# Kernel tuning notes

Hardware: AMD Instinct MI355X
Metric: run time of the kernel (lower is better)

Reference implementation:

```python
import jax, jax.numpy as jnp
import numpy as np

WIDE = 15
PAD = (WIDE - 1) // 2
FREQS = np.array([1., 2., 3., 4., 5., 6.], dtype=np.float32)  # wave_base_ml frequencies


def _lstm_dir(x, wih, whh, b):
    # x: [B,T,F]; wih: [4H,F]; whh: [4H,H]; b: [4H] (b_ih+b_hh fused)
    H = whh.shape[1]
    xg = jnp.einsum('btf,gf->btg', x, wih) + b  # precompute input projections
    def step(carry, xt):
        h, c = carry
        g = xt + h @ whh.T
        i, f, gg, o = jnp.split(g, 4, axis=-1)  # torch gate order i,f,g,o
        c = jax.nn.sigmoid(f) * c + jax.nn.sigmoid(i) * jnp.tanh(gg)
        h = jax.nn.sigmoid(o) * jnp.tanh(c)
        return (h, c), h
    h0 = jnp.zeros((x.shape[0], H), x.dtype)
    _, hs = jax.lax.scan(step, (h0, h0), jnp.swapaxes(xg, 0, 1))
    return jnp.swapaxes(hs, 0, 1)


def _bn(x, g, b, eps=1e-5):
    # training-mode BatchNorm1d over (N, L) per channel; x: [B,C,L]
    m = jnp.mean(x, axis=(0, 2), keepdims=True)
    v = jnp.var(x, axis=(0, 2), keepdims=True)
    return (x - m) * jax.lax.rsqrt(v + eps) * g[None, :, None] + b[None, :, None]


def _conv1d(x, w, b):
    y = jax.lax.conv_general_dilated(x, w, (1,), 'VALID', dimension_numbers=('NCH', 'OIH', 'NCH'))
    return y + b[None, :, None]


def _haar(x):
    s = 0.7071067811865476
    return (x[..., ::2] + x[..., 1::2]) * s, (x[..., ::2] - x[..., 1::2]) * s


def _forward(x, lstm_wif, lstm_whf, lstm_bf, lstm_wir, lstm_whr, lstm_br, base_w, base_b,
             g1, be1, g2, be2, g3, be3, g4, be4, g5, be5,
             w2, b2, w3, b3, w4, b4, w5, b5, fcw, fcb):
    xt = jnp.swapaxes(x, 1, 2)  # [B,T,F]
    fwd = _lstm_dir(xt, lstm_wif, lstm_whf, lstm_bf)
    bwd = _lstm_dir(xt[:, ::-1], lstm_wir, lstm_whr, lstm_br)[:, ::-1]
    X = jnp.swapaxes(jnp.concatenate([fwd, bwd], axis=-1), 1, 2)  # [B,C,T], C=2*dim
    B, C, T = X.shape
    Xp = jnp.pad(X, ((0, 0), (0, 0), (PAD, PAD)))
    # shared sliding windows [B,C,T,WIDE] used both for scale conv and Furi_conv
    Xwin = jnp.stack([Xp[..., k:k + T] for k in range(WIDE)], axis=-1)
    offs = (jnp.arange(WIDE, dtype=X.dtype) - PAD) / WIDE
    outs = []
    for ii in range(len(FREQS)):
        scales = jax.nn.relu(jnp.einsum('bctk,k->bct', Xwin, base_w[ii]) + base_b[ii])
        # per-position cosine Fourier basis generated from the learned scales
        bases = jnp.cos((2.0 * np.pi * FREQS[ii]) * scales[..., None] * offs)  # [B,C,T,WIDE]
        o = jnp.sum(Xwin * bases, axis=-1)  # position-dependent (dynamic) conv
        sqrs = jnp.sqrt((jnp.trunc(scales * WIDE) + 1.0) / (WIDE + 2) * 2.0)
        outs.append(o / sqrs)
    wave = jnp.stack(outs, axis=1).reshape(B, -1, T)  # [B, n_waves*C, T] (wave-major, matches torch cat+view)
    out = _bn(wave, g1, be1)
    out = _bn(jax.nn.relu(_conv1d(out, w2, b2)), g2, be2)
    out = _bn(jax.nn.relu(_conv1d(out, w3, b3)), g3, be3)
    out_back = out  # [B, V_dim, L3]
    out = _bn(jax.nn.relu(_conv1d(out, w4, b4)), g4, be4)  # [B,16,L3-2]
    # 4-level Haar DWT; 5 subbands upsampled to L3, averaged over channels
    a1, d1 = _haar(out_back); a2, d2 = _haar(a1); a3, d3 = _haar(a2); a4, d4 = _haar(a3)
    L3 = out_back.shape[-1]
    bands = [jnp.repeat(bb, L3 // bb.shape[-1], axis=-1) for bb in (a4, d4, d3, d2, d1)]
    dwt = jnp.stack([bb.mean(axis=1) for bb in bands], axis=1)  # [B,5,L3]
    odwt = _bn(jax.nn.relu(_conv1d(dwt, w5, b5)), g5, be5)  # [B,16,L3-2]
    out = jnp.concatenate([out, odwt], axis=-1)
    out = out.mean(axis=-1)  # AdaptiveAvgPool1d(1) + squeeze
    return out @ fcw.T + fcb


def setup_inputs() -> dict:
    key = jax.random.key(0)
    ks = iter(jax.random.split(key, 40))
    def p(shape, s=0.05):
        return jax.random.normal(next(ks), shape, jnp.float32) * s
    B, F, T, DIM, NW, Vd = 32, 64, 518, 64, 6, 32
    C = 2 * DIM
    return {
        'x': jax.random.normal(next(ks), (B, F, T), jnp.float32),
        'lstm_wif': p((4 * DIM, F)), 'lstm_whf': p((4 * DIM, DIM)), 'lstm_bf': p((4 * DIM,)),
        'lstm_wir': p((4 * DIM, F)), 'lstm_whr': p((4 * DIM, DIM)), 'lstm_br': p((4 * DIM,)),
        'base_w': p((NW, WIDE)), 'base_b': p((NW,)),
        'g1': jnp.ones((C * NW,)), 'be1': jnp.zeros((C * NW,)),
        'g2': jnp.ones((128,)), 'be2': jnp.zeros((128,)),
        'g3': jnp.ones((Vd,)), 'be3': jnp.zeros((Vd,)),
        'g4': jnp.ones((16,)), 'be4': jnp.zeros((16,)),
        'g5': jnp.ones((16,)), 'be5': jnp.zeros((16,)),
        'w2': p((128, C * NW, 3)), 'b2': p((128,)),
        'w3': p((Vd, 128, 5)), 'b3': p((Vd,)),
        'w4': p((16, Vd, 3)), 'b4': p((16,)),
        'w5': p((16, 5, 3)), 'b5': p((16,)),
        'fcw': p((10, 16)), 'fcb': p((10,)),
    }


def reference(x, lstm_wif, lstm_whf, lstm_bf, lstm_wir, lstm_whr, lstm_br, base_w, base_b,
              g1, be1, g2, be2, g3, be3, g4, be4, g5, be5,
              w2, b2, w3, b3, w4, b4, w5, b5, fcw, fcb):
    return _forward(x, lstm_wif, lstm_whf, lstm_bf, lstm_wir, lstm_whr, lstm_br, base_w, base_b,
                    g1, be1, g2, be2, g3, be3, g4, be4, g5, be5,
                    w2, b2, w3, b3, w4, b4, w5, b5, fcw, fcb)
```

## Files before the change

kernel.cpp:

```cpp
#include <hip/hip_runtime.h>
#include <math.h>

#define B_     32
#define F_     64
#define T_     518
#define HID    64
#define GATES  256
#define CCH    128
#define NWAVE  6
#define WCH    768
#define L2_    516
#define L3_    512
#define L4_    510

__device__ __forceinline__ float frcp(float x) { return __builtin_amdgcn_rcpf(x); }
__device__ __forceinline__ float fsigmoid(float x) { return frcp(1.f + __expf(-x)); }
__device__ __forceinline__ float ftanh(float x) { return 1.f - 2.f * frcp(1.f + __expf(2.f * x)); }

__global__ void xg_kernel(const float* __restrict__ x,
                          const float* __restrict__ wif, const float* __restrict__ bf,
                          const float* __restrict__ wir, const float* __restrict__ br,
                          float* __restrict__ xg_f, float* __restrict__ xg_r,
                          float* __restrict__ stats) {
    if (blockIdx.x == 0 && blockIdx.y == 0) {
        for (int i = threadIdx.x; i < 2 * WCH; i += 256) stats[i] = 0.f;
    }
    const int tid = threadIdx.x;
    const int wv  = tid >> 7;
    const int g2  = tid & 1;
    const int r   = (tid >> 1) & 63;
    const int g   = (2 * wv + g2) * 64 + r;
    const int b   = blockIdx.y;
    const int t0  = blockIdx.x * 8;
    float4 wa[16], wb[16];
    const float4* w0 = (const float4*)(wif + g * F_);
    const float4* w1 = (const float4*)(wir + g * F_);
#pragma unroll
    for (int i = 0; i < 16; ++i) { wa[i] = w0[i]; wb[i] = w1[i]; }
    const float bfv = bf[g], brv = br[g];
    for (int tt = 0; tt < 8; ++tt) {
        const int t = t0 + tt;
        if (t >= T_) break;
        const float* xp = x + (size_t)b * F_ * T_ + t;
        float a0 = bfv, a1 = brv;
#pragma unroll
        for (int i = 0; i < 16; ++i) {
            float x0 = xp[(i * 4 + 0) * T_];
            float x1 = xp[(i * 4 + 1) * T_];
            float x2 = xp[(i * 4 + 2) * T_];
            float x3 = xp[(i * 4 + 3) * T_];
            a0 += wa[i].x * x0 + wa[i].y * x1 + wa[i].z * x2 + wa[i].w * x3;
            a1 += wb[i].x * x0 + wb[i].y * x1 + wb[i].z * x2 + wb[i].w * x3;
        }
        const size_t o = ((size_t)b * T_ + t) * GATES + tid;
        xg_f[o] = a0;
        xg_r[o] = a1;
    }
}

__global__ __launch_bounds__(128, 1) void lstm_kernel(
        const float* __restrict__ xgi_f, const float* __restrict__ xgi_r,
        const float* __restrict__ whf, const float* __restrict__ whr,
        float* __restrict__ X) {
    const int dir = blockIdx.x & 1;
    const int b   = blockIdx.x >> 1;
    const float* xg  = (dir ? xgi_r : xgi_f) + (size_t)b * T_ * GATES;
    const float* whh = dir ? whr : whf;
    const int tid = threadIdx.x;
    const int r   = tid & 63;
    const int w   = tid >> 6;

    float4 wA[16], wB[16];
    {
        const float4* pA = (const float4*)(whh + (size_t)((2 * w) * HID + r) * HID);
        const float4* pB = (const float4*)(whh + (size_t)((2 * w + 1) * HID + r) * HID);
#pragma unroll
        for (int i = 0; i < 16; ++i) { wA[i] = pA[i]; wB[i] = pB[i]; }
    }

    __shared__ __align__(16) float hs[2][HID];
    __shared__ __align__(16) float gbuf[2][HID][4];
    hs[w][r] = 0.f;
    float c = 0.f;
    float* Xrow = X + ((size_t)(b * CCH + dir * HID + r)) * T_;

    int t = dir ? (T_ - 1) : 0;
    const int step = dir ? -1 : 1;
    const float2* xg2 = (const float2*)xg;
    float2 q0 = xg2[((size_t)t * 2 + w) * 64 + r];
    float2 q1 = xg2[((size_t)(t + step) * 2 + w) * 64 + r];

    for (int s = 0; s < T_; ++s) {
        float4 a0 = {q0.x, 0.f, 0.f, 0.f};
        float4 a1 = {q0.y, 0.f, 0.f, 0.f};
        const float4* h4p = (const float4*)hs[w];
#pragma unroll
        for (int i = 0; i < 16; ++i) {
            const float4 h4 = h4p[i];
            a0.x = fmaf(wA[i].x, h4.x, a0.x); a0.y = fmaf(wA[i].y, h4.y, a0.y);
            a0.z = fmaf(wA[i].z, h4.z, a0.z); a0.w = fmaf(wA[i].w, h4.w, a0.w);
            a1.x = fmaf(wB[i].x, h4.x, a1.x); a1.y = fmaf(wB[i].y, h4.y, a1.y);
            a1.z = fmaf(wB[i].z, h4.z, a1.z); a1.w = fmaf(wB[i].w, h4.w, a1.w);
        }
        const float gA = (a0.x + a0.y) + (a0.z + a0.w);
        const float gB = (a1.x + a1.y) + (a1.z + a1.w);
        const int buf = s & 1;
        *(float2*)&gbuf[buf][r][2 * w] = make_float2(gA, gB);

        int tp = t + 2 * step;
        tp = tp < 0 ? 0 : (tp >= T_ ? T_ - 1 : tp);
        const float2 qn = xg2[((size_t)tp * 2 + w) * 64 + r];

        asm volatile("s_waitcnt lgkmcnt(0)" ::: "memory");
        __builtin_amdgcn_s_barrier();

        const float4 g4 = *(const float4*)gbuf[buf][r];
        const float si = fsigmoid(g4.x);
        const float sf = fsigmoid(g4.y);
        const float so = fsigmoid(g4.w);
        c = sf * c + si * ftanh(g4.z);
        const float h = so * ftanh(c);

        hs[w][r] = h;
        if (w == 0) Xrow[t] = h;
        q0 = q1; q1 = qn;
        t += step;
    }
}

__global__ void wave_kernel(const float* __restrict__ X,
                            const float* __restrict__ bw, const float* __restrict__ bb,
                            float* __restrict__ wave, float* __restrict__ stats) {
    const int b = blockIdx.z, c = blockIdx.y;
    const int t0 = blockIdx.x * 256;
    const int tid = threadIdx.x;
    __shared__ float xs[256 + 14];
    __shared__ float bws[NWAVE][16];
    __shared__ float bbs[NWAVE];
    __shared__ float red[4][12];
    const float* xrow = X + ((size_t)(b * CCH + c)) * T_;
    for (int i = tid; i < 270; i += 256) {
        int tt = t0 - 7 + i;
        xs[i] = (tt >= 0 && tt < T_) ? xrow[tt] : 0.f;
    }
    if (tid < NWAVE * 15) bws[tid / 15][tid % 15] = bw[tid];
    if (tid < NWAVE) bbs[tid] = bb[tid];
    __syncthreads();
    const int t = t0 + tid;
    float ls[NWAVE], lq[NWAVE];
#pragma unroll
    for (int ii = 0; ii < NWAVE; ++ii) { ls[ii] = 0.f; lq[ii] = 0.f; }
    if (t < T_) {
        float win[15];
#pragma unroll
        for (int k = 0; k < 15; ++k) win[k] = xs[tid + k];
        float e[8];
        e[0] = win[7];
#pragma unroll
        for (int m = 1; m < 8; ++m) e[m] = win[7 - m] + win[7 + m];
        const float c0 = 6.28318530717958647692f / 15.f;
#pragma unroll
        for (int ii = 0; ii < NWAVE; ++ii) {
            float sc = bbs[ii];
#pragma unroll
            for (int k = 0; k < 15; ++k) sc += win[k] * bws[ii][k];
            sc = fmaxf(sc, 0.f);
            const float phi = c0 * (float)(ii + 1) * sc;
            float o = e[0];
#pragma unroll
            for (int m = 1; m < 8; ++m) o += e[m] * __cosf(phi * (float)m);
            const float q = (truncf(sc * 15.f) + 1.f) * (2.f / 17.f);
            const float val = o * rsqrtf(q);
            wave[((size_t)(b * WCH + ii * CCH + c)) * T_ + t] = val;
            ls[ii] = val;
            lq[ii] = val * val;
        }
    }
#pragma unroll
    for (int off = 32; off > 0; off >>= 1) {
#pragma unroll
        for (int ii = 0; ii < NWAVE; ++ii) {
            ls[ii] += __shfl_down(ls[ii], off);
            lq[ii] += __shfl_down(lq[ii], off);
        }
    }
    if ((tid & 63) == 0) {
        const int w = tid >> 6;
#pragma unroll
        for (int ii = 0; ii < NWAVE; ++ii) { red[w][ii] = ls[ii]; red[w][6 + ii] = lq[ii]; }
    }
    __syncthreads();
    if (tid < 12) {
        const float a = red[0][tid] + red[1][tid] + red[2][tid] + red[3][tid];
        const int ii = tid % 6;
        const int ch = ii * CCH + c;
        atomicAdd(&stats[(tid >= 6 ? WCH : 0) + ch], a);
    }
}

__global__ void bn1_finalize_kernel(const float* __restrict__ stats,
                                    float* __restrict__ mean, float* __restrict__ rstd) {
    const int c = threadIdx.x;
    const float n = (float)(B_ * T_);
    const float m = stats[c] / n;
    const float v = stats[WCH + c] / n - m * m;
    mean[c] = m;
    rstd[c] = rsqrtf(v + 1e-5f);
}

__global__ void bn_stats_kernel(const float* __restrict__ x, int Bn, int C, int L,
                                float* __restrict__ mean, float* __restrict__ rstd) {
    const int c = blockIdx.x;
    const int tid = threadIdx.x;
    float s = 0.f, s2 = 0.f;
    for (int b = 0; b < Bn; ++b) {
        const float* row = x + ((size_t)b * C + c) * L;
        for (int l = tid; l < L; l += 256) { float v = row[l]; s += v; s2 += v * v; }
    }
#pragma unroll
    for (int off = 32; off > 0; off >>= 1) { s += __shfl_down(s, off); s2 += __shfl_down(s2, off); }
    __shared__ float ss[4], ss2[4];
    if ((tid & 63) == 0) { ss[tid >> 6] = s; ss2[tid >> 6] = s2; }
    __syncthreads();
    if (tid == 0) {
        float S = ss[0] + ss[1] + ss[2] + ss[3];
        float S2 = ss2[0] + ss2[1] + ss2[2] + ss2[3];
        float n = (float)(Bn * L);
        float m = S / n;
        float v = S2 / n - m * m;
        mean[c] = m;
        rstd[c] = rsqrtf(v + 1e-5f);
    }
}

__global__ void bn_apply_row_kernel(float* __restrict__ x, const float* __restrict__ mean,
                                    const float* __restrict__ rstd, const float* __restrict__ g,
                                    const float* __restrict__ be, int C, int L) {
    const int row = blockIdx.x;
    const int c = row % C;
    const float sc = rstd[c] * g[c];
    const float sh = be[c] - mean[c] * sc;
    float* p = x + (size_t)row * L;
    for (int l = threadIdx.x; l < L; l += 256) p[l] = p[l] * sc + sh;
}

__global__ void conv2_kernel(const float* __restrict__ in, const float* __restrict__ w,
                             const float* __restrict__ bias, float* __restrict__ out) {
    const int t = blockIdx.x * 256 + threadIdx.x;
    const int o0 = blockIdx.y * 8;
    const int b = blockIdx.z;
    if (t >= L2_) return;
    float acc[8];
#pragma unroll
    for (int j = 0; j < 8; ++j) acc[j] = bias[o0 + j];
    const float* inb = in + (size_t)b * WCH * T_ + t;
    const float* wb = w + (size_t)o0 * WCH * 3;
    for (int c = 0; c < WCH; ++c) {
        float x0 = inb[c * T_], x1 = inb[c * T_ + 1], x2 = inb[c * T_ + 2];
        const float* wc = wb + c * 3;
#pragma unroll
        for (int j = 0; j < 8; ++j) {
            const float* wj = wc + (size_t)j * WCH * 3;
            acc[j] += x0 * wj[0] + x1 * wj[1] + x2 * wj[2];
        }
    }
    const size_t ob = ((size_t)b * 128 + o0) * L2_ + t;
#pragma unroll
    for (int j = 0; j < 8; ++j) out[ob + (size_t)j * L2_] = fmaxf(acc[j], 0.f);
}

__global__ void conv3_kernel(const float* __restrict__ in, const float* __restrict__ w,
                             const float* __restrict__ bias, float* __restrict__ out) {
    const int t = blockIdx.x * 256 + threadIdx.x;
    const int o0 = blockIdx.y * 8;
    const int b = blockIdx.z;
    if (t >= L3_) return;
    float acc[8];
#pragma unroll
    for (int j = 0; j < 8; ++j) acc[j] = bias[o0 + j];
    const float* inb = in + (size_t)b * 128 * L2_ + t;
    const float* wb = w + (size_t)o0 * 128 * 5;
    for (int c = 0; c < 128; ++c) {
        float x0 = inb[c * L2_], x1 = inb[c * L2_ + 1], x2 = inb[c * L2_ + 2];
        float x3 = inb[c * L2_ + 3], x4 = inb[c * L2_ + 4];
        const float* wc = wb + c * 5;
#pragma unroll
        for (int j = 0; j < 8; ++j) {
            const float* wj = wc + (size_t)j * 128 * 5;
            acc[j] += x0 * wj[0] + x1 * wj[1] + x2 * wj[2] + x3 * wj[3] + x4 * wj[4];
        }
    }
    const size_t ob = ((size_t)b * 32 + o0) * L3_ + t;
#pragma unroll
    for (int j = 0; j < 8; ++j) out[ob + (size_t)j * L3_] = fmaxf(acc[j], 0.f);
}

__global__ void conv4_kernel(const float* __restrict__ in, const float* __restrict__ w,
                             const float* __restrict__ bias, float* __restrict__ out) {
    const int t = blockIdx.x * 256 + threadIdx.x;
    const int o = blockIdx.y;
    const int b = blockIdx.z;
    if (t >= L4_) return;
    float acc = bias[o];
    const float* inb = in + (size_t)b * 32 * L3_ + t;
    const float* wo = w + (size_t)o * 32 * 3;
    for (int c = 0; c < 32; ++c) {
        acc += inb[c * L3_] * wo[c * 3] + inb[c * L3_ + 1] * wo[c * 3 + 1] +
               inb[c * L3_ + 2] * wo[c * 3 + 2];
    }
    out[((size_t)b * 16 + o) * L4_ + t] = fmaxf(acc, 0.f);
}

__global__ __launch_bounds__(512) void dwt_conv5_kernel(const float* __restrict__ y3,
                                                        const float* __restrict__ w5,
                                                        const float* __restrict__ b5,
                                                        float* __restrict__ y5) {
    const int b = blockIdx.x, l = threadIdx.x;
    __shared__ float cm[L3_];
    __shared__ float bands[5][L3_];
    __shared__ float w5s[240];
    __shared__ float b5s[16];
    float s = 0.f;
    for (int ch = 0; ch < 32; ++ch) s += y3[((size_t)b * 32 + ch) * L3_ + l];
    cm[l] = s * (1.f / 32.f);
    if (l < 240) w5s[l] = w5[l];
    if (l < 16) b5s[l] = b5[l];
    __syncthreads();
    const float s1 = 0.70710678118654752440f;
    const float s2c = 0.5f;
    const float s3 = 0.35355339059327378f;
    const float s4 = 0.25f;
    const int b16 = l & ~15, b8 = l & ~7, b4v = l & ~3, b2v = l & ~1;
    float sa = 0.f, sb = 0.f;
#pragma unroll
    for (int i = 0; i < 8; ++i) { sa += cm[b16 + i]; sb += cm[b16 + 8 + i]; }
    bands[0][l] = (sa + sb) * s4;
    bands[1][l] = (sa - sb) * s4;
    float ta = 0.f, tb = 0.f;
#pragma unroll
    for (int i = 0; i < 4; ++i) { ta += cm[b8 + i]; tb += cm[b8 + 4 + i]; }
    bands[2][l] = (ta - tb) * s3;
    bands[3][l] = (cm[b4v] + cm[b4v + 1] - cm[b4v + 2] - cm[b4v + 3]) * s2c;
    bands[4][l] = (cm[b2v] - cm[b2v + 1]) * s1;
    __syncthreads();
    if (l < L4_) {
        float in3[5][3];
#pragma unroll
        for (int c = 0; c < 5; ++c) {
            in3[c][0] = bands[c][l]; in3[c][1] = bands[c][l + 1]; in3[c][2] = bands[c][l + 2];
        }
#pragma unroll
        for (int o = 0; o < 16; ++o) {
            float acc = b5s[o];
#pragma unroll
            for (int c = 0; c < 5; ++c) {
                const float* wp = &w5s[(o * 5 + c) * 3];
                acc += in3[c][0] * wp[0] + in3[c][1] * wp[1] + in3[c][2] * wp[2];
            }
            y5[((size_t)b * 16 + o) * L4_ + l] = fmaxf(acc, 0.f);
        }
    }
}

__global__ __launch_bounds__(512) void tail_final_kernel(
        const float* __restrict__ y4, const float* __restrict__ y5,
        const float* __restrict__ g4, const float* __restrict__ be4,
        const float* __restrict__ g5, const float* __restrict__ be5,
        const float* __restrict__ fcw, const float* __restrict__ fcb,
        float* __restrict__ out) {
    const int p = threadIdx.x;
    const int b = p >> 4, ch = p & 15;
    const float2* p4 = (const float2*)(y4 + ((size_t)(b * 16 + ch)) * L4_);
    const float2* p5 = (const float2*)(y5 + ((size_t)(b * 16 + ch)) * L4_);
    float s4 = 0.f, q4 = 0.f, s5 = 0.f, q5 = 0.f;
    for (int i = 0; i < L4_ / 2; ++i) {
        float2 a = p4[i], bb2 = p5[i];
        s4 += a.x + a.y;  q4 += a.x * a.x + a.y * a.y;
        s5 += bb2.x + bb2.y; q5 += bb2.x * bb2.x + bb2.y * bb2.y;
    }
    __shared__ float S4[512], Q4[512], S5[512], Q5[512];
    __shared__ float M4[16], R4[16], M5[16], R5[16];
    __shared__ float pool[B_][16];
    S4[p] = s4; Q4[p] = q4; S5[p] = s5; Q5[p] = q5;
    __syncthreads();
    if (p < 16) {
        float ts = 0.f, tq = 0.f, us = 0.f, uq = 0.f;
        for (int bb = 0; bb < B_; ++bb) {
            ts += S4[bb * 16 + p]; tq += Q4[bb * 16 + p];
            us += S5[bb * 16 + p]; uq += Q5[bb * 16 + p];
        }
        const float n = (float)(B_ * L4_);
        float m = ts / n; M4[p] = m; R4[p] = rsqrtf(tq / n - m * m + 1e-5f);
        m = us / n;       M5[p] = m; R5[p] = rsqrtf(uq / n - m * m + 1e-5f);
    }
    __syncthreads();
    {
        const float mm4 = s4 / (float)L4_, mm5 = s5 / (float)L4_;
        const float v4 = (mm4 - M4[ch]) * R4[ch] * g4[ch] + be4[ch];
        const float v5 = (mm5 - M5[ch]) * R5[ch] * g5[ch] + be5[ch];
        pool[b][ch] = 0.5f * (v4 + v5);
    }
    __syncthreads();
    if (p < B_ * 10) {
        const int bb = p / 10, row = p - bb * 10;
        float a = fcb[row];
#pragma unroll
        for (int c = 0; c < 16; ++c) a += pool[bb][c] * fcw[row * 16 + c];
        out[bb * 10 + row] = a;
    }
}

extern "C" void kernel_launch(void* const* d_in, const int* in_sizes, int n_in,
                              void* d_out, int out_size, void* d_ws, size_t ws_size,
                              hipStream_t stream) {
    (void)in_sizes; (void)n_in; (void)out_size; (void)ws_size;
    const float* x   = (const float*)d_in[0];
    const float* wif = (const float*)d_in[1];
    const float* whf = (const float*)d_in[2];
    const float* bf  = (const float*)d_in[3];
    const float* wir = (const float*)d_in[4];
    const float* whr = (const float*)d_in[5];
    const float* br  = (const float*)d_in[6];
    const float* bw  = (const float*)d_in[7];
    const float* bb  = (const float*)d_in[8];
    const float* g1  = (const float*)d_in[9];  const float* be1 = (const float*)d_in[10];
    const float* g2  = (const float*)d_in[11]; const float* be2 = (const float*)d_in[12];
    const float* g3  = (const float*)d_in[13]; const float* be3 = (const float*)d_in[14];
    const float* g4  = (const float*)d_in[15]; const float* be4 = (const float*)d_in[16];
    const float* g5  = (const float*)d_in[17]; const float* be5 = (const float*)d_in[18];
    const float* w2  = (const float*)d_in[19]; const float* b2  = (const float*)d_in[20];
    const float* w3  = (const float*)d_in[21]; const float* b3  = (const float*)d_in[22];
    const float* w4  = (const float*)d_in[23]; const float* b4  = (const float*)d_in[24];
    const float* w5  = (const float*)d_in[25]; const float* b5  = (const float*)d_in[26];
    const float* fcw = (const float*)d_in[27]; const float* fcb = (const float*)d_in[28];
    float* out = (float*)d_out;
    float* ws  = (float*)d_ws;

    float* xg_f  = ws;
    float* xg_r  = ws + 4243456;
    float* wave  = ws;
    float* X     = ws + 12730368;
    float* y2    = ws + 14852096;
    float* y3    = ws + 16965632;
    float* y4    = ws + 17489920;
    float* y5    = ws + 17751040;
    float* stats = ws + 18012160;
    float* m1 = ws + 18013696; float* r1 = m1 + 768;
    float* m2 = r1 + 768;      float* r2 = m2 + 128;
    float* m3 = r2 + 128;      float* r3 = m3 + 32;

    xg_kernel<<<dim3(65, 32), 256, 0, stream>>>(x, wif, bf, wir, br, xg_f, xg_r, stats);
    lstm_kernel<<<dim3(64), 128, 0, stream>>>(xg_f, xg_r, whf, whr, X);
    wave_kernel<<<dim3(3, CCH, B_), 256, 0, stream>>>(X, bw, bb, wave, stats);
    bn1_finalize_kernel<<<dim3(1), 768, 0, stream>>>(stats, m1, r1);
    bn_apply_row_kernel<<<dim3(B_ * WCH), 256, 0, stream>>>(wave, m1, r1, g1, be1, WCH, T_);
    conv2_kernel<<<dim3(3, 16, B_), 256, 0, stream>>>(wave, w2, b2, y2);
    bn_stats_kernel<<<dim3(128), 256, 0, stream>>>(y2, B_, 128, L2_, m2, r2);
    bn_apply_row_kernel<<<dim3(B_ * 128), 256, 0, stream>>>(y2, m2, r2, g2, be2, 128, L2_);
    conv3_kernel<<<dim3(2, 4, B_), 256, 0, stream>>>(y2, w3, b3, y3);
    bn_stats_kernel<<<dim3(32), 256, 0, stream>>>(y3, B_, 32, L3_, m3, r3);
    bn_apply_row_kernel<<<dim3(B_ * 32), 256, 0, stream>>>(y3, m3, r3, g3, be3, 32, L3_);
    conv4_kernel<<<dim3(2, 16, B_), 256, 0, stream>>>(y3, w4, b4, y4);
    dwt_conv5_kernel<<<dim3(B_), 512, 0, stream>>>(y3, w5, b5, y5);
    tail_final_kernel<<<dim3(1), 512, 0, stream>>>(y4, y5, g4, be4, g5, be5, fcw, fcb, out);
}
```

Measured before the change: 1.079 ms.

## Fold BatchNorm affine into following conv weights instead of in-place apply passes

Removes the three in-place BatchNorm apply passes over the wave, y2 and y3 tensors. The per-channel scale is folded into transposed copies of the next conv's weights and the shift into its bias, using small fold kernels. Conv kernels are regridded with the batch on the x axis. conv2 now computes 16 outputs per thread and conv4 all 16, both reading output-contiguous transposed weights. The DWT kernel applies the BN3 affine inline. The cost is extra tiny launches and more registers per thread in conv2/conv4. Borders are safe because the convs use VALID padding.

```diff
diff --git a/kernel.cpp b/kernel.cpp
--- a/kernel.cpp
+++ b/kernel.cpp
@@ -233,61 +233,123 @@
     }
 }
 
-__global__ void bn_apply_row_kernel(float* __restrict__ x, const float* __restrict__ mean,
-                                    const float* __restrict__ rstd, const float* __restrict__ g,
-                                    const float* __restrict__ be, int C, int L) {
-    const int row = blockIdx.x;
-    const int c = row % C;
-    const float sc = rstd[c] * g[c];
-    const float sh = be[c] - mean[c] * sc;
-    float* p = x + (size_t)row * L;
-    for (int l = threadIdx.x; l < L; l += 256) p[l] = p[l] * sc + sh;
-}
-
-__global__ void conv2_kernel(const float* __restrict__ in, const float* __restrict__ w,
-                             const float* __restrict__ bias, float* __restrict__ out) {
-    const int t = blockIdx.x * 256 + threadIdx.x;
-    const int o0 = blockIdx.y * 8;
-    const int b = blockIdx.z;
+__global__ void bnfold2_kernel(const float* __restrict__ w2, const float* __restrict__ b2,
+                               const float* __restrict__ m1, const float* __restrict__ r1,
+                               const float* __restrict__ g1, const float* __restrict__ be1,
+                               float* __restrict__ w2t, float* __restrict__ b2t) {
+    const int o = blockIdx.x, tid = threadIdx.x;
+    float part = 0.f;
+    for (int idx = tid; idx < WCH * 3; idx += 256) {
+        const int c = idx / 3;
+        const float sc = r1[c] * g1[c];
+        const float sh = be1[c] - m1[c] * sc;
+        const float wv = w2[(size_t)o * (WCH * 3) + idx];
+        w2t[(size_t)idx * 128 + o] = wv * sc;
+        part += wv * sh;
+    }
+#pragma unroll
+    for (int off = 32; off > 0; off >>= 1) part += __shfl_down(part, off);
+    __shared__ float red[4];
+    if ((tid & 63) == 0) red[tid >> 6] = part;
+    __syncthreads();
+    if (tid == 0) b2t[o] = b2[o] + red[0] + red[1] + red[2] + red[3];
+}
+
+__global__ void bnfold3_kernel(const float* __restrict__ w3, const float* __restrict__ b3,
+                               const float* __restrict__ m2, const float* __restrict__ r2,
+                               const float* __restrict__ g2, const float* __restrict__ be2,
+                               float* __restrict__ w3t, float* __restrict__ b3t) {
+    const int o = blockIdx.x, tid = threadIdx.x;
+    float part = 0.f;
+    for (int idx = tid; idx < 128 * 5; idx += 256) {
+        const int c = idx / 5;
+        const float sc = r2[c] * g2[c];
+        const float sh = be2[c] - m2[c] * sc;
+        const float wv = w3[(size_t)o * 640 + idx];
+        w3t[(size_t)idx * 32 + o] = wv * sc;
+        part += wv * sh;
+    }
+#pragma unroll
+    for (int off = 32; off > 0; off >>= 1) part += __shfl_down(part, off);
+    __shared__ float red[4];
+    if ((tid & 63) == 0) red[tid >> 6] = part;
+    __syncthreads();
+    if (tid == 0) b3t[o] = b3[o] + red[0] + red[1] + red[2] + red[3];
+}
+
+__global__ void bnfold4_kernel(const float* __restrict__ w4, const float* __restrict__ b4,
+                               const float* __restrict__ m3, const float* __restrict__ r3,
+                               const float* __restrict__ g3, const float* __restrict__ be3,
+                               float* __restrict__ w4t, float* __restrict__ b4t,
+                               float* __restrict__ bnp3) {
+    const int o = blockIdx.x, tid = threadIdx.x;
+    float part = 0.f;
+    if (tid < 96) {
+        const int c = tid / 3;
+        const float sc = r3[c] * g3[c];
+        const float sh = be3[c] - m3[c] * sc;
+        const float wv = w4[(size_t)o * 96 + tid];
+        w4t[(size_t)tid * 16 + o] = wv * sc;
+        part = wv * sh;
+    }
+    if (o == 0 && tid >= 96) {
+        const int ch = tid - 96;
+        const float sc = r3[ch] * g3[ch];
+        bnp3[ch] = sc;
+        bnp3[32 + ch] = be3[ch] - m3[ch] * sc;
+    }
+#pragma unroll
+    for (int off = 32; off > 0; off >>= 1) part += __shfl_down(part, off);
+    __shared__ float red[2];
+    if ((tid & 63) == 0) red[tid >> 6] = part;
+    __syncthreads();
+    if (tid == 0) b4t[o] = b4[o] + red[0] + red[1];
+}
+
+__global__ __launch_bounds__(256) void conv2_kernel(
+        const float* __restrict__ in, const float* __restrict__ wt,
+        const float* __restrict__ bt, float* __restrict__ out) {
+    const int b  = blockIdx.x;
+    const int t  = blockIdx.y * 256 + threadIdx.x;
+    const int o0 = blockIdx.z * 16;
     if (t >= L2_) return;
+    float acc[16];
+#pragma unroll
+    for (int j = 0; j < 16; ++j) acc[j] = bt[o0 + j];
+    const float* inb = in + (size_t)b * WCH * T_ + t;
+    for (int c = 0; c < WCH; ++c) {
+        const float x0 = inb[c * T_], x1 = inb[c * T_ + 1], x2 = inb[c * T_ + 2];
+        const float* wc = wt + (size_t)c * 384 + o0;
+#pragma unroll
+        for (int j = 0; j < 16; ++j)
+            acc[j] = fmaf(x0, wc[j], fmaf(x1, wc[128 + j], fmaf(x2, wc[256 + j], acc[j])));
+    }
+    const size_t ob = ((size_t)b * 128 + o0) * L2_ + t;
+#pragma unroll
+    for (int j = 0; j < 16; ++j) out[ob + (size_t)j * L2_] = fmaxf(acc[j], 0.f);
+}
+
+__global__ __launch_bounds__(256) void conv3_kernel(
+        const float* __restrict__ in, const float* __restrict__ wt,
+        const float* __restrict__ bt, float* __restrict__ out) {
+    const int b  = blockIdx.x;
+    const int t  = blockIdx.y * 256 + threadIdx.x;
+    const int o0 = blockIdx.z * 8;
     float acc[8];
 #pragma unroll
-    for (int j = 0; j < 8; ++j) acc[j] = bias[o0 + j];
-    const float* inb = in + (size_t)b * WCH * T_ + t;
-    const float* wb = w + (size_t)o0 * WCH * 3;
-    for (int c = 0; c < WCH; ++c) {
-        float x0 = inb[c * T_], x1 = inb[c * T_ + 1], x2 = inb[c * T_ + 2];
-        const float* wc = wb + c * 3;
+    for (int j = 0; j < 8; ++j) acc[j] = bt[o0 + j];
+    const float* inb = in + (size_t)b * 128 * L2_ + t;
+    for (int c = 0; c < 128; ++c) {
+        const float x0 = inb[c * L2_], x1 = inb[c * L2_ + 1], x2 = inb[c * L2_ + 2];
+        const float x3 = inb[c * L2_ + 3], x4 = inb[c * L2_ + 4];
+        const float* wc = wt + (size_t)c * 160 + o0;
 #pragma unroll
         for (int j = 0; j < 8; ++j) {
-            const float* wj = wc + (size_t)j * WCH * 3;
-            acc[j] += x0 * wj[0] + x1 * wj[1] + x2 * wj[2];
-        }
-    }
-    const size_t ob = ((size_t)b * 128 + o0) * L2_ + t;
-#pragma unroll
-    for (int j = 0; j < 8; ++j) out[ob + (size_t)j * L2_] = fmaxf(acc[j], 0.f);
-}
-
-__global__ void conv3_kernel(const float* __restrict__ in, const float* __restrict__ w,
-                             const float* __restrict__ bias, float* __restrict__ out) {
-    const int t = blockIdx.x * 256 + threadIdx.x;
-    const int o0 = blockIdx.y * 8;
-    const int b = blockIdx.z;
-    if (t >= L3_) return;
-    float acc[8];
-#pragma unroll
-    for (int j = 0; j < 8; ++j) acc[j] = bias[o0 + j];
-    const float* inb = in + (size_t)b * 128 * L2_ + t;
-    const float* wb = w + (size_t)o0 * 128 * 5;
-    for (int c = 0; c < 128; ++c) {
-        float x0 = inb[c * L2_], x1 = inb[c * L2_ + 1], x2 = inb[c * L2_ + 2];
-        float x3 = inb[c * L2_ + 3], x4 = inb[c * L2_ + 4];
-        const float* wc = wb + c * 5;
-#pragma unroll
-        for (int j = 0; j < 8; ++j) {
-            const float* wj = wc + (size_t)j * 128 * 5;
-            acc[j] += x0 * wj[0] + x1 * wj[1] + x2 * wj[2] + x3 * wj[3] + x4 * wj[4];
+            float a = fmaf(x0, wc[j], acc[j]);
+            a = fmaf(x1, wc[32 + j], a);
+            a = fmaf(x2, wc[64 + j], a);
+            a = fmaf(x3, wc[96 + j], a);
+            acc[j] = fmaf(x4, wc[128 + j], a);
         }
     }
     const size_t ob = ((size_t)b * 32 + o0) * L3_ + t;
@@ -295,36 +357,50 @@
     for (int j = 0; j < 8; ++j) out[ob + (size_t)j * L3_] = fmaxf(acc[j], 0.f);
 }
 
-__global__ void conv4_kernel(const float* __restrict__ in, const float* __restrict__ w,
-                             const float* __restrict__ bias, float* __restrict__ out) {
-    const int t = blockIdx.x * 256 + threadIdx.x;
-    const int o = blockIdx.y;
-    const int b = blockIdx.z;
+__global__ __launch_bounds__(256) void conv4_kernel(
+        const float* __restrict__ in, const float* __restrict__ wt,
+        const float* __restrict__ bt, float* __restrict__ out) {
+    const int b = blockIdx.x;
+    const int t = blockIdx.y * 256 + threadIdx.x;
     if (t >= L4_) return;
-    float acc = bias[o];
+    float acc[16];
+#pragma unroll
+    for (int j = 0; j < 16; ++j) acc[j] = bt[j];
     const float* inb = in + (size_t)b * 32 * L3_ + t;
-    const float* wo = w + (size_t)o * 32 * 3;
     for (int c = 0; c < 32; ++c) {
-        acc += inb[c * L3_] * wo[c * 3] + inb[c * L3_ + 1] * wo[c * 3 + 1] +
-               inb[c * L3_ + 2] * wo[c * 3 + 2];
-    }
-    out[((size_t)b * 16 + o) * L4_ + t] = fmaxf(acc, 0.f);
+        const float x0 = inb[c * L3_], x1 = inb[c * L3_ + 1], x2 = inb[c * L3_ + 2];
+        const float* wc = wt + (size_t)c * 48;
+#pragma unroll
+        for (int j = 0; j < 16; ++j)
+            acc[j] = fmaf(x0, wc[j], fmaf(x1, wc[16 + j], fmaf(x2, wc[32 + j], acc[j])));
+    }
+    const size_t ob = ((size_t)b * 16) * L4_ + t;
+#pragma unroll
+    for (int j = 0; j < 16; ++j) out[ob + (size_t)j * L4_] = fmaxf(acc[j], 0.f);
 }
 
 __global__ __launch_bounds__(512) void dwt_conv5_kernel(const float* __restrict__ y3,
                                                         const float* __restrict__ w5,
                                                         const float* __restrict__ b5,
+                                                        const float* __restrict__ bnp3,
                                                         float* __restrict__ y5) {
     const int b = blockIdx.x, l = threadIdx.x;
     __shared__ float cm[L3_];
     __shared__ float bands[5][L3_];
     __shared__ float w5s[240];
     __shared__ float b5s[16];
-    float s = 0.f;
-    for (int ch = 0; ch < 32; ++ch) s += y3[((size_t)b * 32 + ch) * L3_ + l];
-    cm[l] = s * (1.f / 32.f);
+    __shared__ float sc3s[32], sh3s[32];
     if (l < 240) w5s[l] = w5[l];
     if (l < 16) b5s[l] = b5[l];
+    if (l >= 256 && l < 288) sc3s[l - 256] = bnp3[l - 256];
+    if (l >= 288 && l < 320) sh3s[l - 288] = bnp3[32 + (l - 288)];
+    __syncthreads();
+    float s = 0.f, shs = 0.f;
+    for (int ch = 0; ch < 32; ++ch) {
+        s = fmaf(y3[((size_t)b * 32 + ch) * L3_ + l], sc3s[ch], s);
+        shs += sh3s[ch];
+    }
+    cm[l] = (s + shs) * (1.f / 32.f);
     __syncthreads();
     const float s1 = 0.70710678118654752440f;
     const float s2c = 0.5f;
@@ -448,19 +524,26 @@
     float* m1 = ws + 18013696; float* r1 = m1 + 768;
     float* m2 = r1 + 768;      float* r2 = m2 + 128;
     float* m3 = r2 + 128;      float* r3 = m3 + 32;
+    float* w2t  = X;
+    float* b2t  = X + 294912;
+    float* w3t  = X + 295040;
+    float* b3t  = X + 315520;
+    float* w4t  = X + 315552;
+    float* b4t  = X + 317088;
+    float* bnp3 = X + 317104;
 
     xg_kernel<<<dim3(65, 32), 256, 0, stream>>>(x, wif, bf, wir, br, xg_f, xg_r, stats);
     lstm_kernel<<<dim3(64), 128, 0, stream>>>(xg_f, xg_r, whf, whr, X);
     wave_kernel<<<dim3(3, CCH, B_), 256, 0, stream>>>(X, bw, bb, wave, stats);
     bn1_finalize_kernel<<<dim3(1), 768, 0, stream>>>(stats, m1, r1);
-    bn_apply_row_kernel<<<dim3(B_ * WCH), 256, 0, stream>>>(wave, m1, r1, g1, be1, WCH, T_);
-    conv2_kernel<<<dim3(3, 16, B_), 256, 0, stream>>>(wave, w2, b2, y2);
+    bnfold2_kernel<<<dim3(128), 256, 0, stream>>>(w2, b2, m1, r1, g1, be1, w2t, b2t);
+    conv2_kernel<<<dim3(32, 3, 8), 256, 0, stream>>>(wave, w2t, b2t, y2);
     bn_stats_kernel<<<dim3(128), 256, 0, stream>>>(y2, B_, 128, L2_, m2, r2);
-    bn_apply_row_kernel<<<dim3(B_ * 128), 256, 0, stream>>>(y2, m2, r2, g2, be2, 128, L2_);
-    conv3_kernel<<<dim3(2, 4, B_), 256, 0, stream>>>(y2, w3, b3, y3);
+    bnfold3_kernel<<<dim3(32), 256, 0, stream>>>(w3, b3, m2, r2, g2, be2, w3t, b3t);
+    conv3_kernel<<<dim3(32, 2, 4), 256, 0, stream>>>(y2, w3t, b3t, y3);
     bn_stats_kernel<<<dim3(32), 256, 0, stream>>>(y3, B_, 32, L3_, m3, r3);
-    bn_apply_row_kernel<<<dim3(B_ * 32), 256, 0, stream>>>(y3, m3, r3, g3, be3, 32, L3_);
-    conv4_kernel<<<dim3(2, 16, B_), 256, 0, stream>>>(y3, w4, b4, y4);
-    dwt_conv5_kernel<<<dim3(B_), 512, 0, stream>>>(y3, w5, b5, y5);
+    bnfold4_kernel<<<dim3(16), 128, 0, stream>>>(w4, b4, m3, r3, g3, be3, w4t, b4t, bnp3);
+    conv4_kernel<<<dim3(32, 2), 256, 0, stream>>>(y3, w4t, b4t, y4);
+    dwt_conv5_kernel<<<dim3(B_), 512, 0, stream>>>(y3, w5, b5, bnp3, y5);
     tail_final_kernel<<<dim3(1), 512, 0, stream>>>(y4, y5, g4, be4, g5, be5, fcw, fcb, out);
 }
```

After: 1.023 ms. 5.2% less time.
